# Kernel optimization log

Measured on AMD Instinct MI355X. Metric: run time of the kernel, lower is better.

## Reference

```python
import jax, jax.numpy as jnp
import numpy as np

N = 8192
IN_F = 256
OUT_F = 256


def setup_inputs() -> dict:
    key = jax.random.key(0)
    k_v, k_adj, k1, k2, k3, kb = jax.random.split(key, 6)
    stdv = 1.0 / np.sqrt(OUT_F)
    V = jax.random.normal(k_v, (N, IN_F), dtype=jnp.float32)
    adj = jax.random.randint(k_adj, (N, N), 0, 4, dtype=jnp.int32)
    w1 = jax.random.uniform(k1, (IN_F, OUT_F), jnp.float32, -stdv, stdv)
    w2 = jax.random.uniform(k2, (IN_F, OUT_F), jnp.float32, -stdv, stdv)
    w3 = jax.random.uniform(k3, (IN_F, OUT_F), jnp.float32, -stdv, stdv)
    bias = jax.random.uniform(kb, (OUT_F,), jnp.float32, -stdv, stdv)
    return {"V": V, "adj": adj, "w1": w1, "w2": w2, "w3": w3, "bias": bias}


def reference(V, adj, w1, w2, w3, bias):
    # typed relational GCN: for each edge type k in {1,2,3},
    # aggregate (adj==k) @ (V @ wk), then sum and add bias
    o1 = jnp.matmul((adj == 1).astype(jnp.float32), jnp.matmul(V, w1))
    o2 = jnp.matmul((adj == 2).astype(jnp.float32), jnp.matmul(V, w2))
    o3 = jnp.matmul((adj == 3).astype(jnp.float32), jnp.matmul(V, w3))
    return o1 + o2 + o3 + bias
```

## Files before the change

### kernel.cpp

```cpp
#include <hip/hip_runtime.h>

typedef __attribute__((ext_vector_type(4))) float f32x4;
typedef __attribute__((ext_vector_type(16))) float f32x16;
typedef __attribute__((ext_vector_type(4))) unsigned short u16x4;
typedef __attribute__((ext_vector_type(4))) int i32x4;
typedef __attribute__((ext_vector_type(8))) __bf16 bf16x8;

union FragAB {
  u16x4 u[2];
  i32x4 v;
  bf16x8 f;
};

static __device__ __forceinline__ unsigned short f2bf(float x) {
  union { float f; unsigned u; } v;
  v.f = x;
  unsigned r = v.u + 0x7FFFu + ((v.u >> 16) & 1u);
  return (unsigned short)(r >> 16);
}

#define NN 8192

__global__ __launch_bounds__(256) void k_prep(
    const int* __restrict__ adj, const float* __restrict__ V,
    const float* __restrict__ w1, const float* __restrict__ w2,
    const float* __restrict__ w3, const float* __restrict__ bias,
    unsigned char* __restrict__ adj2b, unsigned short* __restrict__ Vbp,
    unsigned short* __restrict__ Wbp, float* __restrict__ out) {
  int t = blockIdx.x * 256 + threadIdx.x;
  int nT = gridDim.x * 256;
  for (int g = t; g < 16777216; g += nT) {
    i32x4 a = *(const i32x4*)(adj + (size_t)g * 4);
    adj2b[g] = (unsigned char)((a.x & 3) | ((a.y & 3) << 2) |
                               ((a.z & 3) << 4) | ((a.w & 3) << 6));
  }
  for (int g = t; g < 524288; g += nT) {
    int f = g * 4;
    int row = f >> 8, kcol = f & 255;
    f32x4 x = *(const f32x4*)(V + (size_t)f);
    u16x4 h;
    h.x = f2bf(x.x); h.y = f2bf(x.y); h.z = f2bf(x.z); h.w = f2bf(x.w);
    *(u16x4*)(Vbp + (size_t)(kcol >> 3) * 65536 + (size_t)row * 8 + (kcol & 7)) = h;
  }
  for (int e = t; e < 65536; e += nT) {
    int k = e >> 8, n = e & 255;
    Wbp[(size_t)(k >> 3) * 6144 + (size_t)(0 * 256 + n) * 8 + (k & 7)] = f2bf(w1[e]);
  }
  for (int e = t; e < 65536; e += nT) {
    int k = e >> 8, n = e & 255;
    Wbp[(size_t)(k >> 3) * 6144 + (size_t)(1 * 256 + n) * 8 + (k & 7)] = f2bf(w2[e]);
  }
  for (int e = t; e < 65536; e += nT) {
    int k = e >> 8, n = e & 255;
    Wbp[(size_t)(k >> 3) * 6144 + (size_t)(2 * 256 + n) * 8 + (k & 7)] = f2bf(w3[e]);
  }
  for (int g = t; g < 524288; g += nT) {
    *(f32x4*)(out + (size_t)g * 4) = *(const f32x4*)(bias + ((g * 4) & 255));
  }
}

__global__ __launch_bounds__(256) void k_transform(
    const unsigned short* __restrict__ Vbp, const unsigned short* __restrict__ Wbp,
    unsigned short* __restrict__ Bp) {
  int bx = blockIdx.x;
  int rb = bx & 127, nb = bx >> 7;
  int tid = threadIdx.x, lane = tid & 63;
  int wv = tid >> 6;
  int wr = wv >> 1, wc = wv & 1;
  int q = lane >> 4, l16 = lane & 15;

  f32x4 acc[2][4];
#pragma unroll
  for (int i = 0; i < 2; i++)
#pragma unroll
    for (int j = 0; j < 4; j++) acc[i][j] = (f32x4)0.0f;

  int r0 = rb * 64 + wr * 32 + l16;
  int n0 = nb * 128 + wc * 64 + l16;
  const unsigned short* av = Vbp + (size_t)q * 65536 + (size_t)r0 * 8;
  const unsigned short* bv = Wbp + (size_t)q * 6144 + (size_t)n0 * 8;

#pragma unroll 2
  for (int kk = 0; kk < 256; kk += 32) {
    FragAB af[2], bf[4];
#pragma unroll
    for (int mt = 0; mt < 2; mt++)
      af[mt].v = *(const i32x4*)(av + (size_t)(kk >> 3) * 65536 + mt * 128);
#pragma unroll
    for (int nt = 0; nt < 4; nt++)
      bf[nt].v = *(const i32x4*)(bv + (size_t)(kk >> 3) * 6144 + nt * 128);
#pragma unroll
    for (int mt = 0; mt < 2; mt++)
#pragma unroll
      for (int nt = 0; nt < 4; nt++)
        acc[mt][nt] = __builtin_amdgcn_mfma_f32_16x16x32_bf16(
            af[mt].f, bf[nt].f, acc[mt][nt], 0, 0, 0);
  }
#pragma unroll
  for (int mt = 0; mt < 2; mt++)
#pragma unroll
    for (int nt = 0; nt < 4; nt++) {
      int n = n0 + nt * 16;
      int ty = n >> 8, nn = n & 255;
      int j0 = rb * 64 + wr * 32 + mt * 16 + q * 4;
      u16x4 hv;
      hv.x = f2bf(acc[mt][nt].x);
      hv.y = f2bf(acc[mt][nt].y);
      hv.z = f2bf(acc[mt][nt].z);
      hv.w = f2bf(acc[mt][nt].w);
      size_t idx = (size_t)ty * 2097152 + (size_t)(j0 >> 4) * 4096 + nn * 16 + (j0 & 15);
      *(u16x4*)(Bp + idx) = hv;
    }
}

__global__ __launch_bounds__(256, 2) void k_agg(const unsigned* __restrict__ adj2,
                                                const unsigned short* __restrict__ Bp,
                                                float* __restrict__ out) {
  int bx = blockIdx.x;
  int ks = bx & 7, rb = bx >> 3;
  int tid = threadIdx.x, lane = tid & 63;
  int wv = tid >> 6;
  int wm = wv >> 1, wn = wv & 1;
  int q = lane >> 5, l32 = lane & 31;
  int qsh = q << 4;

  f32x16 acc[2][4];
#pragma unroll
  for (int mt = 0; mt < 2; mt++)
#pragma unroll
    for (int nt = 0; nt < 4; nt++) acc[mt][nt] = (f32x16)0.0f;

  int r0 = rb * 128 + wm * 64 + l32;
  const unsigned* ap0 = adj2 + (size_t)r0 * 512 + ks * 64;
  const unsigned* ap1 = ap0 + 32 * 512;

  int nbase = (wn * 128 + l32) * 16 + q * 8;
  const unsigned short* bb[3][2];
#pragma unroll
  for (int ty = 0; ty < 3; ty++)
#pragma unroll
    for (int kh = 0; kh < 2; kh++)
      bb[ty][kh] = Bp + (size_t)ty * 2097152 + ((size_t)ks * 64 + kh) * 4096 + nbase;

  unsigned long long c0 = *(const unsigned long long*)ap0;
  unsigned long long c1 = *(const unsigned long long*)ap1;

  for (int step = 0; step < 32; ++step) {
    unsigned long long nx0 = 0, nx1 = 0;
    if (step < 31) {
      nx0 = *(const unsigned long long*)(ap0 + 2 * (step + 1));
      nx1 = *(const unsigned long long*)(ap1 + 2 * (step + 1));
    }
    FragAB bv0[3][4];
#pragma unroll
    for (int ty = 0; ty < 3; ty++)
#pragma unroll
      for (int nt = 0; nt < 4; nt++)
        bv0[ty][nt].v = *(const i32x4*)(bb[ty][0] + nt * 512);
    {
      unsigned w0 = (unsigned)c0 >> qsh;
      unsigned w1 = (unsigned)c1 >> qsh;
#pragma unroll
      for (int ty = 0; ty < 3; ty++) {
        FragAB A0, A1;
#pragma unroll
        for (int d = 0; d < 4; d++) {
          unsigned p00 = (w0 >> (4 * d)) & 3u, p01 = (w0 >> (4 * d + 2)) & 3u;
          unsigned p10 = (w1 >> (4 * d)) & 3u, p11 = (w1 >> (4 * d + 2)) & 3u;
          A0.v[d] = (int)((p00 == (unsigned)(ty + 1) ? 0x3F80u : 0u) |
                          (p01 == (unsigned)(ty + 1) ? 0x3F800000u : 0u));
          A1.v[d] = (int)((p10 == (unsigned)(ty + 1) ? 0x3F80u : 0u) |
                          (p11 == (unsigned)(ty + 1) ? 0x3F800000u : 0u));
        }
#pragma unroll
        for (int nt = 0; nt < 4; nt++) {
          acc[0][nt] = __builtin_amdgcn_mfma_f32_32x32x16_bf16(
              A0.f, bv0[ty][nt].f, acc[0][nt], 0, 0, 0);
          acc[1][nt] = __builtin_amdgcn_mfma_f32_32x32x16_bf16(
              A1.f, bv0[ty][nt].f, acc[1][nt], 0, 0, 0);
        }
      }
    }
    FragAB bv1[3][4];
#pragma unroll
    for (int ty = 0; ty < 3; ty++)
#pragma unroll
      for (int nt = 0; nt < 4; nt++)
        bv1[ty][nt].v = *(const i32x4*)(bb[ty][1] + nt * 512);
    {
      unsigned w0 = (unsigned)(c0 >> 32) >> qsh;
      unsigned w1 = (unsigned)(c1 >> 32) >> qsh;
#pragma unroll
      for (int ty = 0; ty < 3; ty++) {
        FragAB A0, A1;
#pragma unroll
        for (int d = 0; d < 4; d++) {
          unsigned p00 = (w0 >> (4 * d)) & 3u, p01 = (w0 >> (4 * d + 2)) & 3u;
          unsigned p10 = (w1 >> (4 * d)) & 3u, p11 = (w1 >> (4 * d + 2)) & 3u;
          A0.v[d] = (int)((p00 == (unsigned)(ty + 1) ? 0x3F80u : 0u) |
                          (p01 == (unsigned)(ty + 1) ? 0x3F800000u : 0u));
          A1.v[d] = (int)((p10 == (unsigned)(ty + 1) ? 0x3F80u : 0u) |
                          (p11 == (unsigned)(ty + 1) ? 0x3F800000u : 0u));
        }
#pragma unroll
        for (int nt = 0; nt < 4; nt++) {
          acc[0][nt] = __builtin_amdgcn_mfma_f32_32x32x16_bf16(
              A0.f, bv1[ty][nt].f, acc[0][nt], 0, 0, 0);
          acc[1][nt] = __builtin_amdgcn_mfma_f32_32x32x16_bf16(
              A1.f, bv1[ty][nt].f, acc[1][nt], 0, 0, 0);
        }
      }
    }
#pragma unroll
    for (int ty = 0; ty < 3; ty++)
#pragma unroll
      for (int kh = 0; kh < 2; kh++) bb[ty][kh] += 8192;
    c0 = nx0;
    c1 = nx1;
  }
#pragma unroll
  for (int mt = 0; mt < 2; mt++)
#pragma unroll
    for (int nt = 0; nt < 4; nt++) {
      int col = wn * 128 + nt * 32 + l32;
      int rowb = rb * 128 + wm * 64 + mt * 32 + 4 * q;
#pragma unroll
      for (int r = 0; r < 16; r++) {
        int row = rowb + (r & 3) + 8 * (r >> 2);
        atomicAdd(out + (size_t)row * 256 + col, acc[mt][nt][r]);
      }
    }
}

extern "C" void kernel_launch(void* const* d_in, const int* in_sizes, int n_in,
                              void* d_out, int out_size, void* d_ws,
                              size_t ws_size, hipStream_t stream) {
  const float* V = (const float*)d_in[0];
  const int* adj = (const int*)d_in[1];
  const float* w1 = (const float*)d_in[2];
  const float* w2 = (const float*)d_in[3];
  const float* w3 = (const float*)d_in[4];
  const float* bias = (const float*)d_in[5];
  float* out = (float*)d_out;
  unsigned short* Bp = (unsigned short*)d_ws;
  unsigned char* adj2b = (unsigned char*)d_ws + 0xC00000;
  unsigned short* Vbp = (unsigned short*)((char*)d_ws + 0x1C00000);
  unsigned short* Wbp = (unsigned short*)((char*)d_ws + 0x2000000);

  k_prep<<<dim3(2048), dim3(256), 0, stream>>>(adj, V, w1, w2, w3, bias, adj2b,
                                               Vbp, Wbp, out);
  k_transform<<<dim3(768), dim3(256), 0, stream>>>(Vbp, Wbp, Bp);
  k_agg<<<dim3(512), dim3(256), 0, stream>>>((const unsigned*)adj2b, Bp, out);
}
```

Baseline: 499.7 us.

## Software-pipeline B fragment loads through a 3-slot rotating register buffer

Restructures the aggregation inner loop so B fragment global loads for the next (type, k-half) chunk are issued before the MFMAs of the current chunk, using a 3-slot rotating register buffer and a prologue that preloads two chunks across loop iterations. It aims to hide global load latency behind MFMA work instead of loading all 24 fragments and then computing. It cuts live B registers from 24 to 12 fragments, which may also help occupancy, but it adds cross-iteration dependencies that the compiler might reorder or serialize.

```diff
diff --git a/kernel.cpp b/kernel.cpp
--- a/kernel.cpp
+++ b/kernel.cpp
@@ -145,79 +145,69 @@
   unsigned long long c0 = *(const unsigned long long*)ap0;
   unsigned long long c1 = *(const unsigned long long*)ap1;
 
+  FragAB ch[3][4];
+
+#define AGG_ISSUE(SLOT, TY, KH)                                                \
+  {                                                                            \
+    _Pragma("unroll") for (int nt = 0; nt < 4; nt++)                           \
+        ch[SLOT][nt].v = *(const i32x4*)(bb[TY][KH] + nt * 512);               \
+  }
+
+#define AGG_COMPUTE(SLOT, TY, HI)                                              \
+  {                                                                            \
+    unsigned w0 = (unsigned)(HI ? (c0 >> 32) : c0) >> qsh;                     \
+    unsigned w1 = (unsigned)(HI ? (c1 >> 32) : c1) >> qsh;                     \
+    FragAB A0, A1;                                                             \
+    _Pragma("unroll") for (int d = 0; d < 4; d++) {                            \
+      unsigned p00 = (w0 >> (4 * d)) & 3u, p01 = (w0 >> (4 * d + 2)) & 3u;     \
+      unsigned p10 = (w1 >> (4 * d)) & 3u, p11 = (w1 >> (4 * d + 2)) & 3u;     \
+      A0.v[d] = (int)((p00 == (unsigned)(TY + 1) ? 0x3F80u : 0u) |             \
+                      (p01 == (unsigned)(TY + 1) ? 0x3F800000u : 0u));         \
+      A1.v[d] = (int)((p10 == (unsigned)(TY + 1) ? 0x3F80u : 0u) |             \
+                      (p11 == (unsigned)(TY + 1) ? 0x3F800000u : 0u));         \
+    }                                                                          \
+    _Pragma("unroll") for (int nt = 0; nt < 4; nt++) {                         \
+      acc[0][nt] = __builtin_amdgcn_mfma_f32_32x32x16_bf16(                    \
+          A0.f, ch[SLOT][nt].f, acc[0][nt], 0, 0, 0);                          \
+      acc[1][nt] = __builtin_amdgcn_mfma_f32_32x32x16_bf16(                    \
+          A1.f, ch[SLOT][nt].f, acc[1][nt], 0, 0, 0);                          \
+    }                                                                          \
+  }
+
+  AGG_ISSUE(0, 0, 0)
+  AGG_ISSUE(1, 1, 0)
+
   for (int step = 0; step < 32; ++step) {
     unsigned long long nx0 = 0, nx1 = 0;
     if (step < 31) {
       nx0 = *(const unsigned long long*)(ap0 + 2 * (step + 1));
       nx1 = *(const unsigned long long*)(ap1 + 2 * (step + 1));
     }
-    FragAB bv0[3][4];
+    AGG_COMPUTE(0, 0, 0)
+    AGG_ISSUE(2, 2, 0)
+    AGG_COMPUTE(1, 1, 0)
+    AGG_ISSUE(0, 0, 1)
+    AGG_COMPUTE(2, 2, 0)
+    AGG_ISSUE(1, 1, 1)
+    AGG_COMPUTE(0, 0, 1)
+    AGG_ISSUE(2, 2, 1)
 #pragma unroll
     for (int ty = 0; ty < 3; ty++)
 #pragma unroll
-      for (int nt = 0; nt < 4; nt++)
-        bv0[ty][nt].v = *(const i32x4*)(bb[ty][0] + nt * 512);
-    {
-      unsigned w0 = (unsigned)c0 >> qsh;
-      unsigned w1 = (unsigned)c1 >> qsh;
-#pragma unroll
-      for (int ty = 0; ty < 3; ty++) {
-        FragAB A0, A1;
-#pragma unroll
-        for (int d = 0; d < 4; d++) {
-          unsigned p00 = (w0 >> (4 * d)) & 3u, p01 = (w0 >> (4 * d + 2)) & 3u;
-          unsigned p10 = (w1 >> (4 * d)) & 3u, p11 = (w1 >> (4 * d + 2)) & 3u;
-          A0.v[d] = (int)((p00 == (unsigned)(ty + 1) ? 0x3F80u : 0u) |
-                          (p01 == (unsigned)(ty + 1) ? 0x3F800000u : 0u));
-          A1.v[d] = (int)((p10 == (unsigned)(ty + 1) ? 0x3F80u : 0u) |
-                          (p11 == (unsigned)(ty + 1) ? 0x3F800000u : 0u));
-        }
-#pragma unroll
-        for (int nt = 0; nt < 4; nt++) {
-          acc[0][nt] = __builtin_amdgcn_mfma_f32_32x32x16_bf16(
-              A0.f, bv0[ty][nt].f, acc[0][nt], 0, 0, 0);
-          acc[1][nt] = __builtin_amdgcn_mfma_f32_32x32x16_bf16(
-              A1.f, bv0[ty][nt].f, acc[1][nt], 0, 0, 0);
-        }
-      }
-    }
-    FragAB bv1[3][4];
-#pragma unroll
-    for (int ty = 0; ty < 3; ty++)
-#pragma unroll
-      for (int nt = 0; nt < 4; nt++)
-        bv1[ty][nt].v = *(const i32x4*)(bb[ty][1] + nt * 512);
-    {
-      unsigned w0 = (unsigned)(c0 >> 32) >> qsh;
-      unsigned w1 = (unsigned)(c1 >> 32) >> qsh;
-#pragma unroll
-      for (int ty = 0; ty < 3; ty++) {
-        FragAB A0, A1;
-#pragma unroll
-        for (int d = 0; d < 4; d++) {
-          unsigned p00 = (w0 >> (4 * d)) & 3u, p01 = (w0 >> (4 * d + 2)) & 3u;
-          unsigned p10 = (w1 >> (4 * d)) & 3u, p11 = (w1 >> (4 * d + 2)) & 3u;
-          A0.v[d] = (int)((p00 == (unsigned)(ty + 1) ? 0x3F80u : 0u) |
-                          (p01 == (unsigned)(ty + 1) ? 0x3F800000u : 0u));
-          A1.v[d] = (int)((p10 == (unsigned)(ty + 1) ? 0x3F80u : 0u) |
-                          (p11 == (unsigned)(ty + 1) ? 0x3F800000u : 0u));
-        }
-#pragma unroll
-        for (int nt = 0; nt < 4; nt++) {
-          acc[0][nt] = __builtin_amdgcn_mfma_f32_32x32x16_bf16(
-              A0.f, bv1[ty][nt].f, acc[0][nt], 0, 0, 0);
-          acc[1][nt] = __builtin_amdgcn_mfma_f32_32x32x16_bf16(
-              A1.f, bv1[ty][nt].f, acc[1][nt], 0, 0, 0);
-        }
-      }
-    }
-#pragma unroll
-    for (int ty = 0; ty < 3; ty++)
-#pragma unroll
       for (int kh = 0; kh < 2; kh++) bb[ty][kh] += 8192;
+    AGG_COMPUTE(1, 1, 1)
+    if (step < 31) {
+      AGG_ISSUE(0, 0, 0)
+    }
+    AGG_COMPUTE(2, 2, 1)
+    if (step < 31) {
+      AGG_ISSUE(1, 1, 0)
+    }
     c0 = nx0;
     c1 = nx1;
   }
+#undef AGG_ISSUE
+#undef AGG_COMPUTE
 #pragma unroll
   for (int mt = 0; mt < 2; mt++)
 #pragma unroll
```

Result: no change. 491.5 us (-1.6%).
